# Optimization experiments

Measured on AMD Instinct MI355X. Metric: run time of the kernel, lower is better.

## Reference

```python
import jax, jax.numpy as jnp
import numpy as np

BS, LS, NWRD, D, H, NTGT, MC = 32, 512, 100000, 128, 512, 2048, 20
TEMP = 0.5  # gumbel-softmax temperature (self.last_t)
HLOSS_COEF = 0.03


def setup_inputs() -> dict:
    key = jax.random.key(0)
    ks = jax.random.split(key, 12)
    inp_word = jax.random.randint(ks[0], (BS, LS), 0, NWRD, dtype=jnp.int32)
    inp_char = jax.random.randint(ks[1], (BS, LS, MC), 0, 95, dtype=jnp.int32)
    inp_pos = jax.random.randint(ks[2], (BS, LS), 0, 50, dtype=jnp.int32)
    keyword_table = jax.random.bernoulli(ks[3], 0.1, (NWRD,))  # wid in keywords_set
    tgt_ids = jax.random.randint(ks[4], (NTGT,), 0, NWRD, dtype=jnp.int32)
    lut = jax.random.randint(ks[5], (NWRD, MC), 0, 95, dtype=jnp.int32)
    u = jax.random.uniform(ks[6], (BS, LS, NTGT), minval=1e-6, maxval=1.0 - 1e-6)
    gumbel = -jnp.log(-jnp.log(u))  # standard Gumbel(0,1) noise
    W = jax.random.normal(ks[7], (NWRD, D), dtype=jnp.float32) * 0.02
    W1 = jax.random.normal(ks[8], (D, H), dtype=jnp.float32) * (1.0 / np.sqrt(D))
    b1 = jnp.zeros((H,), jnp.float32)
    W2 = jax.random.normal(ks[9], (H, NTGT), dtype=jnp.float32) * (1.0 / np.sqrt(H))
    b2 = jnp.zeros((NTGT,), jnp.float32)
    return dict(inp_word=inp_word, inp_char=inp_char, inp_pos=inp_pos,
                keyword_table=keyword_table, tgt_ids=tgt_ids, lut=lut,
                gumbel=gumbel, W=W, W1=W1, b1=b1, W2=W2, b2=b2)


def reference(inp_word, inp_char, inp_pos, keyword_table, tgt_ids, lut,
              gumbel, W, W1, b1, W2, b2):
    # keyword membership mask (idx in the original; torch gathers only masked
    # spots -- here we compute densely and select with the mask, same math at
    # every masked position, identity elsewhere)
    mask = keyword_table[inp_word]                      # [bs, ls] bool

    x = W[inp_word]                                     # embed: [bs, ls, d]
    hdn = jax.nn.relu(jnp.einsum('bsd,dh->bsh', x, W1) + b1)
    logits = jnp.einsum('bsh,ht->bst', hdn, W2) + b2    # [bs, ls, ntgt]

    # log_p.masked_scatter_(idx, x.max(-1)[0])
    log_p = jnp.where(mask, logits.max(axis=-1), 0.0)

    # hloss: mean entropy over masked spots * 0.03
    lsm = jax.nn.log_softmax(logits, axis=-1)
    ent = -jnp.sum(jnp.exp(lsm) * lsm, axis=-1)         # [bs, ls]
    n_spots = jnp.maximum(mask.sum(), 1)
    loss_h = (ent * mask).sum() / n_spots * HLOSS_COEF

    # gumbel_softmax(x, t): softmax((logits + g) / t)
    sft = jax.nn.softmax((logits + gumbel) / TEMP, axis=-1)  # [bs, ls, ntgt]

    # hard pick mapped through tgtwords, scattered into word
    y = tgt_ids[jnp.argmax(sft, axis=-1)]               # [bs, ls]
    word = jnp.where(mask, y, inp_word)

    # soft embedding: sft @ word_emb_tgt, word_emb_tgt = W[tgt_ids]
    x_emb = jnp.einsum('bst,td->bsd', sft, W[tgt_ids])  # [bs, ls, d]
    word_emb = jnp.where(mask[..., None], x_emb, x)     # scatter into W[word]

    char = lut[word]                                    # word_to_char lookup

    return (mask.astype(jnp.float32), log_p, word, char, word_emb, loss_h)
```

## Files before the change

### kernel.cpp

```cpp
#include <hip/hip_runtime.h>
#include <cstdint>

#define R_TOT 16384
#define T_NT  2048
#define DD    128
#define HH    512
#define MC_   20
#define BR    32
#define STEPS 64
#define NBLK  (R_TOT / BR)

#define MASK_OFF 0
#define LOGP_OFF 16384
#define WORD_OFF 32768
#define CHAR_OFF 49152
#define EMB_OFF  376832
#define LOSS_OFF 2473984

#define X_OFF     0
#define HDN_OFF   2097152
#define HDNB_OFF  10485760
#define WT_OFF    14680064
#define WTT_OFF   14942208
#define W2T_OFF   15073280
#define W2TB_OFF  16121856
#define ENT_OFF   16646144
#define CNT_OFF   16647168

typedef __attribute__((ext_vector_type(8))) short short8v;
typedef __attribute__((ext_vector_type(4))) float f32x4;
typedef unsigned short ushort_t;

__device__ __forceinline__ ushort_t f2bf(float f) {
    union { float f; unsigned int u; } v; v.f = f;
    unsigned int r = v.u + 0x7FFFu + ((v.u >> 16) & 1u);
    return (ushort_t)(r >> 16);
}

__device__ __forceinline__ void stage16(const ushort_t* gsrc, ushort_t* ldst) {
    __builtin_amdgcn_global_load_lds(
        (const __attribute__((address_space(1))) unsigned int*)gsrc,
        (__attribute__((address_space(3))) unsigned int*)ldst, 16, 0, 0);
}

__global__ __launch_bounds__(256) void k1_gather(
    const int* __restrict__ inp_word, const int* __restrict__ tgt_ids,
    const float* __restrict__ W, float* __restrict__ x, float* __restrict__ wtgt)
{
    int row = blockIdx.x * 2 + (threadIdx.x >> 7);
    int d = threadIdx.x & 127;
    if (row < R_TOT) {
        int wsrc = inp_word[row];
        x[(size_t)row * DD + d] = W[(size_t)wsrc * DD + d];
    } else {
        int rr = row - R_TOT;
        if (rr < T_NT) {
            int wsrc = tgt_ids[rr];
            wtgt[(size_t)rr * DD + d] = W[(size_t)wsrc * DD + d];
        }
    }
}

__global__ __launch_bounds__(256) void k1b_wtgtT(
    const float* __restrict__ wtgt, ushort_t* __restrict__ wtgtT)
{
    __shared__ float tile[32][33];
    int tb = blockIdx.x * 32, db = blockIdx.y * 32;
    int lx = threadIdx.x & 31, ly = threadIdx.x >> 5;
    #pragma unroll
    for (int i = 0; i < 32; i += 8)
        tile[ly + i][lx] = wtgt[(size_t)(tb + ly + i) * DD + db + lx];
    __syncthreads();
    #pragma unroll
    for (int i = 0; i < 32; i += 8)
        wtgtT[(size_t)(db + ly + i) * T_NT + tb + lx] = f2bf(tile[lx][ly + i]);
}

__global__ __launch_bounds__(256) void k0_w2t(
    const float* __restrict__ W2, float* __restrict__ W2Tf, ushort_t* __restrict__ W2Tb)
{
    __shared__ float tile[32][33];
    int cb = blockIdx.x * 32, kb = blockIdx.y * 32;
    int lx = threadIdx.x & 31, ly = threadIdx.x >> 5;
    #pragma unroll
    for (int i = 0; i < 32; i += 8)
        tile[ly + i][lx] = W2[(size_t)(kb + ly + i) * T_NT + cb + lx];
    __syncthreads();
    #pragma unroll
    for (int i = 0; i < 32; i += 8) {
        int c = cb + ly + i, k = kb + lx;
        float v = tile[lx][ly + i];
        W2Tf[(size_t)c * HH + k] = v;
        W2Tb[(size_t)c * HH + k] = f2bf(v);
    }
}

__global__ __launch_bounds__(256) void k2_hdn(
    const float* __restrict__ x, const float* __restrict__ W1,
    const float* __restrict__ b1, float* __restrict__ hdn, ushort_t* __restrict__ hdnB)
{
    __shared__ float As[16][64];
    __shared__ float Bs[16][64];
    const int t = threadIdx.x;
    const int bm = blockIdx.x * 64;
    const int bn = blockIdx.y * 64;
    const int tx = t & 15, ty = t >> 4;
    float acc[4][4] = {};
    for (int k0 = 0; k0 < DD; k0 += 16) {
        {
            int m = t >> 2, kq = t & 3;
            float4 v = *(const float4*)(x + (size_t)(bm + m) * DD + k0 + kq * 4);
            As[kq * 4 + 0][m] = v.x; As[kq * 4 + 1][m] = v.y;
            As[kq * 4 + 2][m] = v.z; As[kq * 4 + 3][m] = v.w;
        }
        {
            int k = t >> 4, nq = t & 15;
            *(float4*)(&Bs[k][nq * 4]) =
                *(const float4*)(W1 + (size_t)(k0 + k) * HH + bn + nq * 4);
        }
        __syncthreads();
        #pragma unroll
        for (int k = 0; k < 16; ++k) {
            float a[4], b[4];
            #pragma unroll
            for (int i = 0; i < 4; i++) a[i] = As[k][ty * 4 + i];
            #pragma unroll
            for (int j = 0; j < 4; j++) b[j] = Bs[k][tx * 4 + j];
            #pragma unroll
            for (int i = 0; i < 4; i++)
                #pragma unroll
                for (int j = 0; j < 4; j++)
                    acc[i][j] = fmaf(a[i], b[j], acc[i][j]);
        }
        __syncthreads();
    }
    #pragma unroll
    for (int i = 0; i < 4; i++) {
        int m = bm + ty * 4 + i;
        int n = bn + tx * 4;
        float4 v;
        v.x = fmaxf(acc[i][0] + b1[n + 0], 0.f);
        v.y = fmaxf(acc[i][1] + b1[n + 1], 0.f);
        v.z = fmaxf(acc[i][2] + b1[n + 2], 0.f);
        v.w = fmaxf(acc[i][3] + b1[n + 3], 0.f);
        *(float4*)(hdn + (size_t)m * HH + n) = v;
        ushort4 hb;
        hb.x = f2bf(v.x); hb.y = f2bf(v.y); hb.z = f2bf(v.z); hb.w = f2bf(v.w);
        *(ushort4*)(hdnB + (size_t)m * HH + n) = hb;
    }
}

__global__ __launch_bounds__(256) void k3_fused(
    const ushort_t* __restrict__ hdnB, const float* __restrict__ hdn,
    const ushort_t* __restrict__ W2Tb, const float* __restrict__ W2Tf,
    const float* __restrict__ b2, const float* __restrict__ gumbel,
    const int* __restrict__ inp_word, const int* __restrict__ keyword_table,
    const int* __restrict__ tgt_ids, const int* __restrict__ lut,
    const float* __restrict__ x, const ushort_t* __restrict__ wtgtT,
    float* __restrict__ out, float* __restrict__ entP, float* __restrict__ cntP)
{
    __shared__ ushort_t wS[2][16384];
    __shared__ float pS[2 * 2 * 16 * 36];
    __shared__ float statC1[2 * 16 * 8];
    __shared__ int   candS[BR * 2];
    __shared__ float invs2S[BR], entS[BR];
    __shared__ int   mskS[BR];

    const int t = threadIdx.x;
    const int wid = t >> 6, lane = t & 63;
    const int Mgrp = wid >> 1, Cgrp = wid & 1;
    const int lrow = lane & 15, kgrp = lane >> 4;
    const int row0 = blockIdx.x * BR;
    const int rowA = row0 + Mgrp * 16 + lrow;
    const int c_local = Cgrp * 16 + lrow;

    short8v av[16];
    #pragma unroll
    for (int ks = 0; ks < 16; ++ks)
        av[ks] = *(const short8v*)(hdnB + (size_t)rowA * HH + ks * 32 + kgrp * 8);

    float m_[4], sE_[4], sEl_[4], s2_[4], a1_[4], a2_[4];
    int i1_[4], i2_[4];
    #pragma unroll
    for (int q = 0; q < 4; ++q) {
        m_[q] = -1e30f; sE_[q] = 0.f; sEl_[q] = 0.f; s2_[q] = 0.f;
        a1_[q] = -1e30f; a2_[q] = -1e30f; i1_[q] = 0; i2_[q] = 0;
    }
    f32x4 accpv[4];
    #pragma unroll
    for (int df = 0; df < 4; ++df) accpv[df] = (f32x4){0.f, 0.f, 0.f, 0.f};

    auto stage_tile = [&](int buf, int s_step) {
        const int col0 = s_step * 32;
        #pragma unroll
        for (int i = 0; i < 8; ++i) {
            int slot = wid * 512 + i * 64 + lane;
            int c = slot >> 6, kc = slot & 63;
            const ushort_t* gsrc = W2Tb + (size_t)(col0 + c) * HH + ((kc ^ (c & 7)) << 3);
            stage16(gsrc, &wS[buf][(size_t)(wid * 512 + i * 64) * 8]);
        }
    };

    stage_tile(0, 0);
    __syncthreads();

    const int dbase = Cgrp * 64 + lrow;

    for (int s = 0; s < STEPS; ++s) {
        const int buf = s & 1, par = s & 1;
        const int col = s * 32 + c_local;

        float g4[4];
        #pragma unroll
        for (int q = 0; q < 4; ++q)
            g4[q] = gumbel[(size_t)(row0 + Mgrp * 16 + kgrp * 4 + q) * T_NT + col];
        float b2v = b2[col];
        short8v bvf[4];
        #pragma unroll
        for (int df = 0; df < 4; ++df)
            bvf[df] = *(const short8v*)(wtgtT + (size_t)(dbase + df * 16) * T_NT + s * 32 + kgrp * 8);

        if (s + 1 < STEPS) stage_tile(buf ^ 1, s + 1);

        f32x4 acc = (f32x4){0.f, 0.f, 0.f, 0.f};
        #pragma unroll
        for (int ks = 0; ks < 16; ++ks) {
            int kc = ks * 4 + kgrp;
            const short8v bv = *(const short8v*)&wS[buf][c_local * 512 + ((kc ^ (c_local & 7)) << 3)];
            acc = __builtin_amdgcn_mfma_f32_16x16x32_bf16(av[ks], bv, acc, 0, 0, 0);
        }

        float* pT = &pS[(Mgrp * 2 + par) * 576];
        #pragma unroll
        for (int q = 0; q < 4; ++q) {
            float l = acc[q] + b2v;
            m_[q] = fmaxf(m_[q], l);
            float e1 = __expf(l);
            sE_[q] += e1; sEl_[q] = fmaf(e1, l, sEl_[q]);
            float a = l + g4[q];
            float p = __expf(2.0f * a);
            s2_[q] += p;
            if (a > a1_[q]) { a2_[q] = a1_[q]; i2_[q] = i1_[q]; a1_[q] = a; i1_[q] = col; }
            else if (a > a2_[q]) { a2_[q] = a; i2_[q] = col; }
            pT[(kgrp * 4 + q) * 36 + c_local] = p;
        }

        __syncthreads();

        {
            const float* pr = &pS[(Mgrp * 2 + par) * 576 + lrow * 36 + kgrp * 8];
            float4 pa = *(const float4*)(pr);
            float4 pb = *(const float4*)(pr + 4);
            short8v pav;
            pav[0] = (short)f2bf(pa.x); pav[1] = (short)f2bf(pa.y);
            pav[2] = (short)f2bf(pa.z); pav[3] = (short)f2bf(pa.w);
            pav[4] = (short)f2bf(pb.x); pav[5] = (short)f2bf(pb.y);
            pav[6] = (short)f2bf(pb.z); pav[7] = (short)f2bf(pb.w);
            #pragma unroll
            for (int df = 0; df < 4; ++df)
                accpv[df] = __builtin_amdgcn_mfma_f32_16x16x32_bf16(pav, bvf[df], accpv[df], 0, 0, 0);
        }
    }

    #pragma unroll
    for (int q = 0; q < 4; ++q) {
        #pragma unroll
        for (int mk = 1; mk < 16; mk <<= 1) {
            m_[q] = fmaxf(m_[q], __shfl_xor(m_[q], mk));
            sE_[q] += __shfl_xor(sE_[q], mk);
            sEl_[q] += __shfl_xor(sEl_[q], mk);
            s2_[q] += __shfl_xor(s2_[q], mk);
            float ob1 = __shfl_xor(a1_[q], mk); int oj1 = __shfl_xor(i1_[q], mk);
            float ob2 = __shfl_xor(a2_[q], mk); int oj2 = __shfl_xor(i2_[q], mk);
            if (ob1 > a1_[q] || (ob1 == a1_[q] && oj1 < i1_[q])) {
                if (a1_[q] > ob2 || (a1_[q] == ob2 && i1_[q] < oj2)) { a2_[q] = a1_[q]; i2_[q] = i1_[q]; }
                else { a2_[q] = ob2; i2_[q] = oj2; }
                a1_[q] = ob1; i1_[q] = oj1;
            } else {
                if (ob1 > a2_[q]) { a2_[q] = ob1; i2_[q] = oj1; }
            }
        }
    }

    if (Cgrp == 1 && lrow == 0) {
        #pragma unroll
        for (int q = 0; q < 4; ++q) {
            int r = kgrp * 4 + q;
            float* st = &statC1[(Mgrp * 16 + r) * 8];
            st[0] = m_[q]; st[1] = sE_[q]; st[2] = sEl_[q]; st[3] = s2_[q];
            st[4] = a1_[q]; st[5] = __int_as_float(i1_[q]);
            st[6] = a2_[q]; st[7] = __int_as_float(i2_[q]);
        }
    }
    __syncthreads();

    if (Cgrp == 0) {
        #pragma unroll
        for (int q = 0; q < 4; ++q) {
            int r = kgrp * 4 + q;
            const float* st = &statC1[(Mgrp * 16 + r) * 8];
            float bm = st[0], bsE = st[1], bsEl = st[2], bs2 = st[3];
            float b1v = st[4]; int j1 = __float_as_int(st[5]);
            float b2c = st[6]; int j2 = __float_as_int(st[7]);
            float m = fmaxf(m_[q], bm);
            float sE = sE_[q] + bsE, sEl = sEl_[q] + bsEl, s2 = s2_[q] + bs2;
            float a1 = a1_[q], a2 = a2_[q]; int i1 = i1_[q], i2 = i2_[q];
            if (b1v > a1 || (b1v == a1 && j1 < i1)) {
                if (a1 > b2c || (a1 == b2c && i1 < j2)) { a2 = a1; i2 = i1; }
                else { a2 = b2c; i2 = j2; }
                a1 = b1v; i1 = j1;
            } else {
                if (b1v > a2) { a2 = b1v; i2 = j1; }
            }
            if (lrow == 0) {
                int grow = row0 + Mgrp * 16 + r;
                int w_in = inp_word[grow];
                int msk = keyword_table[w_in] != 0;
                out[MASK_OFF + grow] = msk ? 1.0f : 0.0f;
                out[LOGP_OFF + grow] = msk ? m : 0.0f;
                invs2S[Mgrp * 16 + r] = 1.0f / s2;
                mskS[Mgrp * 16 + r] = msk;
                entS[Mgrp * 16 + r] = msk ? (__logf(sE) - sEl / sE) : 0.0f;
                candS[(Mgrp * 16 + r) * 2 + 0] = i1;
                candS[(Mgrp * 16 + r) * 2 + 1] = i2;
            }
        }
    }
    __syncthreads();

    #pragma unroll
    for (int df = 0; df < 4; ++df) {
        #pragma unroll
        for (int q = 0; q < 4; ++q) {
            int rl = Mgrp * 16 + kgrp * 4 + q;
            int grow = row0 + rl;
            int d = dbase + df * 16;
            float val = accpv[df][q] * invs2S[rl];
            if (!mskS[rl]) val = x[(size_t)grow * DD + d];
            out[EMB_OFF + (size_t)grow * DD + d] = val;
        }
    }

    for (int rr = wid * 8; rr < wid * 8 + 8; ++rr) {
        int grow = row0 + rr;
        int i1 = candS[rr * 2 + 0], i2 = candS[rr * 2 + 1];
        const float* hrow = hdn + (size_t)grow * HH;
        float4 h0 = *(const float4*)(hrow + lane * 8);
        float4 h1 = *(const float4*)(hrow + lane * 8 + 4);
        float v1, v2;
        {
            const float* wrow = W2Tf + (size_t)i1 * HH;
            float4 w0 = *(const float4*)(wrow + lane * 8);
            float4 w1 = *(const float4*)(wrow + lane * 8 + 4);
            float sdot = h0.x*w0.x + h0.y*w0.y + h0.z*w0.z + h0.w*w0.w
                       + h1.x*w1.x + h1.y*w1.y + h1.z*w1.z + h1.w*w1.w;
            #pragma unroll
            for (int mk = 1; mk < 64; mk <<= 1) sdot += __shfl_xor(sdot, mk);
            v1 = sdot + b2[i1] + gumbel[(size_t)grow * T_NT + i1];
        }
        {
            const float* wrow = W2Tf + (size_t)i2 * HH;
            float4 w0 = *(const float4*)(wrow + lane * 8);
            float4 w1 = *(const float4*)(wrow + lane * 8 + 4);
            float sdot = h0.x*w0.x + h0.y*w0.y + h0.z*w0.z + h0.w*w0.w
                       + h1.x*w1.x + h1.y*w1.y + h1.z*w1.z + h1.w*w1.w;
            #pragma unroll
            for (int mk = 1; mk < 64; mk <<= 1) sdot += __shfl_xor(sdot, mk);
            v2 = sdot + b2[i2] + gumbel[(size_t)grow * T_NT + i2];
        }
        int ibest = (v2 > v1 || (v2 == v1 && i2 < i1)) ? i2 : i1;
        int w_in = inp_word[grow];
        int msk = mskS[rr];
        int word = msk ? tgt_ids[ibest] : w_in;
        if (lane == 0) out[WORD_OFF + grow] = (float)word;
        if (lane < MC_)
            out[CHAR_OFF + (size_t)grow * MC_ + lane] = (float)lut[(size_t)word * MC_ + lane];
    }

    if (t == 0) {
        float es = 0.f; int cs = 0;
        #pragma unroll
        for (int r = 0; r < BR; r++) { es += entS[r]; cs += mskS[r]; }
        entP[blockIdx.x] = es;
        cntP[blockIdx.x] = (float)cs;
    }
}

__global__ __launch_bounds__(256) void k4_loss(
    const float* __restrict__ entP, const float* __restrict__ cntP, float* __restrict__ out)
{
    __shared__ float sE[256], sC[256];
    int t = threadIdx.x;
    float e = 0.f, c = 0.f;
    for (int i = t; i < NBLK; i += 256) { e += entP[i]; c += cntP[i]; }
    sE[t] = e; sC[t] = c;
    __syncthreads();
    for (int s = 128; s > 0; s >>= 1) {
        if (t < s) { sE[t] += sE[t + s]; sC[t] += sC[t + s]; }
        __syncthreads();
    }
    if (t == 0) {
        float ns = fmaxf(sC[0], 1.0f);
        out[LOSS_OFF] = 0.03f * sE[0] / ns;
    }
}

extern "C" void kernel_launch(void* const* d_in, const int* in_sizes, int n_in,
                              void* d_out, int out_size, void* d_ws, size_t ws_size,
                              hipStream_t stream) {
    const int* inp_word = (const int*)d_in[0];
    const int* keyword_table = (const int*)d_in[3];
    const int* tgt_ids = (const int*)d_in[4];
    const int* lut = (const int*)d_in[5];
    const float* gumbel = (const float*)d_in[6];
    const float* W = (const float*)d_in[7];
    const float* W1 = (const float*)d_in[8];
    const float* b1 = (const float*)d_in[9];
    const float* W2 = (const float*)d_in[10];
    const float* b2 = (const float*)d_in[11];
    float* out = (float*)d_out;

    float* wsf = (float*)d_ws;
    float* x = wsf + X_OFF;
    float* hdn = wsf + HDN_OFF;
    ushort_t* hdnB = (ushort_t*)(wsf + HDNB_OFF);
    float* wtgt = wsf + WT_OFF;
    ushort_t* wtgtT = (ushort_t*)(wsf + WTT_OFF);
    float* W2Tf = wsf + W2T_OFF;
    ushort_t* W2Tb = (ushort_t*)(wsf + W2TB_OFF);
    float* entP = wsf + ENT_OFF;
    float* cntP = wsf + CNT_OFF;

    k1_gather<<<(R_TOT + T_NT) / 2, 256, 0, stream>>>(inp_word, tgt_ids, W, x, wtgt);
    k1b_wtgtT<<<dim3(T_NT / 32, DD / 32), 256, 0, stream>>>(wtgt, wtgtT);
    k0_w2t<<<dim3(T_NT / 32, HH / 32), 256, 0, stream>>>(W2, W2Tf, W2Tb);
    k2_hdn<<<dim3(R_TOT / 64, HH / 64), 256, 0, stream>>>(x, W1, b1, hdn, hdnB);
    k3_fused<<<NBLK, 256, 0, stream>>>(hdnB, hdn, W2Tb, W2Tf, b2, gumbel,
                                       inp_word, keyword_table, tgt_ids, lut,
                                       x, wtgtT, out, entP, cntP);
    k4_loss<<<1, 256, 0, stream>>>(entP, cntP, out);
}
```

Baseline: 219.5 us.

## Prepack W2 and target embeddings into MFMA fragment layouts for the fused kernel

W2 and the gathered target embeddings are pre-packed in bf16 in the exact per-lane MFMA fragment order. The fused kernel can then stage contiguous tiles and read B fragments directly, without XOR swizzle address math or strided loads. The probability-times-embedding MFMA now runs per warp over its own 16 columns, zero-padding half of each K=32 input. This uses 8 accumulators covering all of D, and the two column-group partials are reduced through shared memory at the end. The logit MFMA chain is also split into four independent accumulators to improve ILP. The trade-off is more registers, wasted MFMA work on the padded inputs, and an extra reduction pass.

```diff
diff --git a/kernel.cpp b/kernel.cpp
--- a/kernel.cpp
+++ b/kernel.cpp
@@ -21,11 +21,11 @@
 #define HDN_OFF   2097152
 #define HDNB_OFF  10485760
 #define WT_OFF    14680064
-#define WTT_OFF   14942208
-#define W2T_OFF   15073280
-#define W2TB_OFF  16121856
-#define ENT_OFF   16646144
-#define CNT_OFF   16647168
+#define WTT4_OFF  14942208
+#define W2T_OFF   15204352
+#define W2P_OFF   16252928
+#define ENT_OFF   16777216
+#define CNT_OFF   16777728
 
 typedef __attribute__((ext_vector_type(8))) short short8v;
 typedef __attribute__((ext_vector_type(4))) float f32x4;
@@ -61,27 +61,33 @@
     }
 }
 
-__global__ __launch_bounds__(256) void k1b_wtgtT(
-    const float* __restrict__ wtgt, ushort_t* __restrict__ wtgtT)
+__global__ __launch_bounds__(256) void k1b_wtgtT4(
+    const float* __restrict__ wtgt, ushort_t* __restrict__ wtgtT4)
+{
+    const int js = blockIdx.x, t = threadIdx.x;
+    #pragma unroll
+    for (int i = 0; i < 4; ++i) {
+        int s = i * 256 + t;
+        int cs = s >> 9, rem = s & 511;
+        int df = rem >> 6, lane = rem & 63;
+        int lrow = lane & 15, kg = lane >> 4;
+        ushort_t* dst = wtgtT4 + (size_t)(((js * 2 + cs) * 8 + df) * 512 + lane * 8);
+        #pragma unroll
+        for (int j = 0; j < 8; ++j) {
+            dst[j] = (j < 4)
+                ? f2bf(wtgt[(size_t)(js * 32 + cs * 16 + kg * 4 + j) * DD + df * 16 + lrow])
+                : (ushort_t)0;
+        }
+    }
+}
+
+__global__ __launch_bounds__(256) void k0_w2t(
+    const float* __restrict__ W2, float* __restrict__ W2Tf, ushort_t* __restrict__ W2p)
 {
     __shared__ float tile[32][33];
-    int tb = blockIdx.x * 32, db = blockIdx.y * 32;
-    int lx = threadIdx.x & 31, ly = threadIdx.x >> 5;
-    #pragma unroll
-    for (int i = 0; i < 32; i += 8)
-        tile[ly + i][lx] = wtgt[(size_t)(tb + ly + i) * DD + db + lx];
-    __syncthreads();
-    #pragma unroll
-    for (int i = 0; i < 32; i += 8)
-        wtgtT[(size_t)(db + ly + i) * T_NT + tb + lx] = f2bf(tile[lx][ly + i]);
-}
-
-__global__ __launch_bounds__(256) void k0_w2t(
-    const float* __restrict__ W2, float* __restrict__ W2Tf, ushort_t* __restrict__ W2Tb)
-{
-    __shared__ float tile[32][33];
-    int cb = blockIdx.x * 32, kb = blockIdx.y * 32;
-    int lx = threadIdx.x & 31, ly = threadIdx.x >> 5;
+    const int js = blockIdx.x, ks = blockIdx.y;
+    const int cb = js * 32, kb = ks * 32;
+    const int lx = threadIdx.x & 31, ly = threadIdx.x >> 5;
     #pragma unroll
     for (int i = 0; i < 32; i += 8)
         tile[ly + i][lx] = W2[(size_t)(kb + ly + i) * T_NT + cb + lx];
@@ -89,9 +95,14 @@
     #pragma unroll
     for (int i = 0; i < 32; i += 8) {
         int c = cb + ly + i, k = kb + lx;
-        float v = tile[lx][ly + i];
-        W2Tf[(size_t)c * HH + k] = v;
-        W2Tb[(size_t)c * HH + k] = f2bf(v);
+        W2Tf[(size_t)c * HH + k] = tile[lx][ly + i];
+    }
+    if (threadIdx.x < 128) {
+        int c = threadIdx.x >> 2, kgrp = threadIdx.x & 3;
+        ushort_t* dst = W2p + (size_t)((js * 16 + ks) * 1024 + (c * 4 + kgrp) * 8);
+        #pragma unroll
+        for (int i = 0; i < 8; ++i)
+            dst[i] = f2bf(tile[kgrp * 8 + i][c]);
     }
 }
 
@@ -152,15 +163,15 @@
 
 __global__ __launch_bounds__(256) void k3_fused(
     const ushort_t* __restrict__ hdnB, const float* __restrict__ hdn,
-    const ushort_t* __restrict__ W2Tb, const float* __restrict__ W2Tf,
+    const ushort_t* __restrict__ W2p, const float* __restrict__ W2Tf,
     const float* __restrict__ b2, const float* __restrict__ gumbel,
     const int* __restrict__ inp_word, const int* __restrict__ keyword_table,
     const int* __restrict__ tgt_ids, const int* __restrict__ lut,
-    const float* __restrict__ x, const ushort_t* __restrict__ wtgtT,
+    const float* __restrict__ x, const ushort_t* __restrict__ wtgtT4,
     float* __restrict__ out, float* __restrict__ entP, float* __restrict__ cntP)
 {
-    __shared__ ushort_t wS[2][16384];
-    __shared__ float pS[2 * 2 * 16 * 36];
+    __shared__ ushort_t wS[2 * 16384];
+    __shared__ float pS[4][16 * 20];
     __shared__ float statC1[2 * 16 * 8];
     __shared__ int   candS[BR * 2];
     __shared__ float invs2S[BR], entS[BR];
@@ -172,12 +183,22 @@
     const int lrow = lane & 15, kgrp = lane >> 4;
     const int row0 = blockIdx.x * BR;
     const int rowA = row0 + Mgrp * 16 + lrow;
-    const int c_local = Cgrp * 16 + lrow;
 
     short8v av[16];
     #pragma unroll
     for (int ks = 0; ks < 16; ++ks)
         av[ks] = *(const short8v*)(hdnB + (size_t)rowA * HH + ks * 32 + kgrp * 8);
+
+    const ushort_t* wb = wS + ((Cgrp * 16 + lrow) * 4 + kgrp) * 8;
+
+    const float* gp0 = gumbel + (size_t)(row0 + Mgrp * 16 + kgrp * 4 + 0) * T_NT + Cgrp * 16 + lrow;
+    const float* gp1 = gp0 + T_NT;
+    const float* gp2 = gp1 + T_NT;
+    const float* gp3 = gp2 + T_NT;
+    const float* b2p = b2 + Cgrp * 16 + lrow;
+    const ushort_t* vtp = wtgtT4 + (size_t)Cgrp * 4096 + lane * 8;
+
+    float* pw = &pS[wid][0];
 
     float m_[4], sE_[4], sEl_[4], s2_[4], a1_[4], a2_[4];
     int i1_[4], i2_[4];
@@ -186,51 +207,51 @@
         m_[q] = -1e30f; sE_[q] = 0.f; sEl_[q] = 0.f; s2_[q] = 0.f;
         a1_[q] = -1e30f; a2_[q] = -1e30f; i1_[q] = 0; i2_[q] = 0;
     }
-    f32x4 accpv[4];
-    #pragma unroll
-    for (int df = 0; df < 4; ++df) accpv[df] = (f32x4){0.f, 0.f, 0.f, 0.f};
-
-    auto stage_tile = [&](int buf, int s_step) {
-        const int col0 = s_step * 32;
-        #pragma unroll
-        for (int i = 0; i < 8; ++i) {
-            int slot = wid * 512 + i * 64 + lane;
-            int c = slot >> 6, kc = slot & 63;
-            const ushort_t* gsrc = W2Tb + (size_t)(col0 + c) * HH + ((kc ^ (c & 7)) << 3);
-            stage16(gsrc, &wS[buf][(size_t)(wid * 512 + i * 64) * 8]);
-        }
-    };
-
-    stage_tile(0, 0);
+    f32x4 accpv[8];
+    #pragma unroll
+    for (int df = 0; df < 8; ++df) accpv[df] = (f32x4){0.f, 0.f, 0.f, 0.f};
+
+    {
+        const ushort_t* src = W2p + t * 8;
+        ushort_t* dst = wS + t * 8;
+        #pragma unroll
+        for (int i = 0; i < 8; ++i) stage16(src + i * 2048, dst + i * 2048);
+    }
     __syncthreads();
 
-    const int dbase = Cgrp * 64 + lrow;
+    int colv = Cgrp * 16 + lrow;
 
     for (int s = 0; s < STEPS; ++s) {
-        const int buf = s & 1, par = s & 1;
-        const int col = s * 32 + c_local;
-
-        float g4[4];
-        #pragma unroll
-        for (int q = 0; q < 4; ++q)
-            g4[q] = gumbel[(size_t)(row0 + Mgrp * 16 + kgrp * 4 + q) * T_NT + col];
-        float b2v = b2[col];
-        short8v bvf[4];
-        #pragma unroll
-        for (int df = 0; df < 4; ++df)
-            bvf[df] = *(const short8v*)(wtgtT + (size_t)(dbase + df * 16) * T_NT + s * 32 + kgrp * 8);
-
-        if (s + 1 < STEPS) stage_tile(buf ^ 1, s + 1);
-
-        f32x4 acc = (f32x4){0.f, 0.f, 0.f, 0.f};
-        #pragma unroll
-        for (int ks = 0; ks < 16; ++ks) {
-            int kc = ks * 4 + kgrp;
-            const short8v bv = *(const short8v*)&wS[buf][c_local * 512 + ((kc ^ (c_local & 7)) << 3)];
-            acc = __builtin_amdgcn_mfma_f32_16x16x32_bf16(av[ks], bv, acc, 0, 0, 0);
-        }
-
-        float* pT = &pS[(Mgrp * 2 + par) * 576];
+        const int buf = s & 1;
+
+        if (s + 1 < STEPS) {
+            const ushort_t* src = W2p + (size_t)(s + 1) * 16384 + t * 8;
+            ushort_t* dst = wS + (buf ^ 1) * 16384 + t * 8;
+            #pragma unroll
+            for (int i = 0; i < 8; ++i) stage16(src + i * 2048, dst + i * 2048);
+        }
+
+        float g0 = *gp0, g1 = *gp1, g2 = *gp2, g3 = *gp3;
+        gp0 += 32; gp1 += 32; gp2 += 32; gp3 += 32;
+        float b2v = *b2p; b2p += 32;
+        short8v bvf[8];
+        #pragma unroll
+        for (int df = 0; df < 8; ++df)
+            bvf[df] = *(const short8v*)(vtp + df * 512);
+        vtp += 8192;
+
+        const ushort_t* wbb = wb + buf * 16384;
+        f32x4 ac0 = (f32x4){0.f,0.f,0.f,0.f}, ac1 = ac0, ac2 = ac0, ac3 = ac0;
+        #pragma unroll
+        for (int ks = 0; ks < 16; ks += 4) {
+            ac0 = __builtin_amdgcn_mfma_f32_16x16x32_bf16(av[ks+0], *(const short8v*)(wbb + (ks+0)*1024), ac0, 0, 0, 0);
+            ac1 = __builtin_amdgcn_mfma_f32_16x16x32_bf16(av[ks+1], *(const short8v*)(wbb + (ks+1)*1024), ac1, 0, 0, 0);
+            ac2 = __builtin_amdgcn_mfma_f32_16x16x32_bf16(av[ks+2], *(const short8v*)(wbb + (ks+2)*1024), ac2, 0, 0, 0);
+            ac3 = __builtin_amdgcn_mfma_f32_16x16x32_bf16(av[ks+3], *(const short8v*)(wbb + (ks+3)*1024), ac3, 0, 0, 0);
+        }
+        f32x4 acc = (ac0 + ac1) + (ac2 + ac3);
+
+        float g4[4] = {g0, g1, g2, g3};
         #pragma unroll
         for (int q = 0; q < 4; ++q) {
             float l = acc[q] + b2v;
@@ -240,26 +261,24 @@
             float a = l + g4[q];
             float p = __expf(2.0f * a);
             s2_[q] += p;
-            if (a > a1_[q]) { a2_[q] = a1_[q]; i2_[q] = i1_[q]; a1_[q] = a; i1_[q] = col; }
-            else if (a > a2_[q]) { a2_[q] = a; i2_[q] = col; }
-            pT[(kgrp * 4 + q) * 36 + c_local] = p;
+            if (a > a1_[q]) { a2_[q] = a1_[q]; i2_[q] = i1_[q]; a1_[q] = a; i1_[q] = colv; }
+            else if (a > a2_[q]) { a2_[q] = a; i2_[q] = colv; }
+            pw[(kgrp * 4 + q) * 20 + lrow] = p;
+        }
+
+        {
+            float4 p4 = *(const float4*)(pw + lrow * 20 + kgrp * 4);
+            short8v pav;
+            pav[0] = (short)f2bf(p4.x); pav[1] = (short)f2bf(p4.y);
+            pav[2] = (short)f2bf(p4.z); pav[3] = (short)f2bf(p4.w);
+            pav[4] = 0; pav[5] = 0; pav[6] = 0; pav[7] = 0;
+            #pragma unroll
+            for (int df = 0; df < 8; ++df)
+                accpv[df] = __builtin_amdgcn_mfma_f32_16x16x32_bf16(pav, bvf[df], accpv[df], 0, 0, 0);
         }
 
         __syncthreads();
-
-        {
-            const float* pr = &pS[(Mgrp * 2 + par) * 576 + lrow * 36 + kgrp * 8];
-            float4 pa = *(const float4*)(pr);
-            float4 pb = *(const float4*)(pr + 4);
-            short8v pav;
-            pav[0] = (short)f2bf(pa.x); pav[1] = (short)f2bf(pa.y);
-            pav[2] = (short)f2bf(pa.z); pav[3] = (short)f2bf(pa.w);
-            pav[4] = (short)f2bf(pb.x); pav[5] = (short)f2bf(pb.y);
-            pav[6] = (short)f2bf(pb.z); pav[7] = (short)f2bf(pb.w);
-            #pragma unroll
-            for (int df = 0; df < 4; ++df)
-                accpv[df] = __builtin_amdgcn_mfma_f32_16x16x32_bf16(pav, bvf[df], accpv[df], 0, 0, 0);
-        }
+        colv += 32;
     }
 
     #pragma unroll
@@ -285,12 +304,19 @@
     if (Cgrp == 1 && lrow == 0) {
         #pragma unroll
         for (int q = 0; q < 4; ++q) {
-            int r = kgrp * 4 + q;
-            float* st = &statC1[(Mgrp * 16 + r) * 8];
+            float* st = &statC1[(Mgrp * 16 + kgrp * 4 + q) * 8];
             st[0] = m_[q]; st[1] = sE_[q]; st[2] = sEl_[q]; st[3] = s2_[q];
             st[4] = a1_[q]; st[5] = __int_as_float(i1_[q]);
             st[6] = a2_[q]; st[7] = __int_as_float(i2_[q]);
         }
+    }
+    float* scr = (float*)wS;
+    if (Cgrp == 1) {
+        #pragma unroll
+        for (int df = 0; df < 8; ++df)
+            #pragma unroll
+            for (int q = 0; q < 4; ++q)
+                scr[Mgrp * 2048 + (kgrp * 4 + q) * 128 + df * 16 + lrow] = accpv[df][q];
     }
     __syncthreads();
 
@@ -300,48 +326,56 @@
             int r = kgrp * 4 + q;
             const float* st = &statC1[(Mgrp * 16 + r) * 8];
             float bm = st[0], bsE = st[1], bsEl = st[2], bs2 = st[3];
-            float b1v = st[4]; int j1 = __float_as_int(st[5]);
-            float b2c = st[6]; int j2 = __float_as_int(st[7]);
+            float ob1 = st[4]; int oj1 = __float_as_int(st[5]);
+            float ob2 = st[6]; int oj2 = __float_as_int(st[7]);
             float m = fmaxf(m_[q], bm);
             float sE = sE_[q] + bsE, sEl = sEl_[q] + bsEl, s2 = s2_[q] + bs2;
             float a1 = a1_[q], a2 = a2_[q]; int i1 = i1_[q], i2 = i2_[q];
-            if (b1v > a1 || (b1v == a1 && j1 < i1)) {
-                if (a1 > b2c || (a1 == b2c && i1 < j2)) { a2 = a1; i2 = i1; }
-                else { a2 = b2c; i2 = j2; }
-                a1 = b1v; i1 = j1;
+            if (ob1 > a1 || (ob1 == a1 && oj1 < i1)) {
+                if (a1 > ob2 || (a1 == ob2 && i1 < oj2)) { a2 = a1; i2 = i1; }
+                else { a2 = ob2; i2 = oj2; }
+                a1 = ob1; i1 = oj1;
             } else {
-                if (b1v > a2) { a2 = b1v; i2 = j1; }
+                if (ob1 > a2) { a2 = ob1; i2 = oj1; }
             }
             if (lrow == 0) {
-                int grow = row0 + Mgrp * 16 + r;
+                int rl = Mgrp * 16 + r;
+                int grow = row0 + rl;
                 int w_in = inp_word[grow];
                 int msk = keyword_table[w_in] != 0;
                 out[MASK_OFF + grow] = msk ? 1.0f : 0.0f;
                 out[LOGP_OFF + grow] = msk ? m : 0.0f;
-                invs2S[Mgrp * 16 + r] = 1.0f / s2;
-                mskS[Mgrp * 16 + r] = msk;
-                entS[Mgrp * 16 + r] = msk ? (__logf(sE) - sEl / sE) : 0.0f;
-                candS[(Mgrp * 16 + r) * 2 + 0] = i1;
-                candS[(Mgrp * 16 + r) * 2 + 1] = i2;
+                invs2S[rl] = 1.0f / s2;
+                mskS[rl] = msk;
+                entS[rl] = msk ? (__logf(sE) - sEl / sE) : 0.0f;
+                candS[rl * 2 + 0] = i1;
+                candS[rl * 2 + 1] = i2;
             }
         }
+        #pragma unroll
+        for (int df = 0; df < 8; ++df)
+            #pragma unroll
+            for (int q = 0; q < 4; ++q)
+                accpv[df][q] += scr[Mgrp * 2048 + (kgrp * 4 + q) * 128 + df * 16 + lrow];
     }
     __syncthreads();
 
-    #pragma unroll
-    for (int df = 0; df < 4; ++df) {
-        #pragma unroll
-        for (int q = 0; q < 4; ++q) {
-            int rl = Mgrp * 16 + kgrp * 4 + q;
-            int grow = row0 + rl;
-            int d = dbase + df * 16;
-            float val = accpv[df][q] * invs2S[rl];
-            if (!mskS[rl]) val = x[(size_t)grow * DD + d];
-            out[EMB_OFF + (size_t)grow * DD + d] = val;
-        }
-    }
-
-    for (int rr = wid * 8; rr < wid * 8 + 8; ++rr) {
+    if (Cgrp == 0) {
+        #pragma unroll
+        for (int df = 0; df < 8; ++df) {
+            #pragma unroll
+            for (int q = 0; q < 4; ++q) {
+                int rl = Mgrp * 16 + kgrp * 4 + q;
+                int grow = row0 + rl;
+                int d = df * 16 + lrow;
+                float val = accpv[df][q] * invs2S[rl];
+                if (!mskS[rl]) val = x[(size_t)grow * DD + d];
+                out[EMB_OFF + (size_t)grow * DD + d] = val;
+            }
+        }
+    }
+
+    for (int rr = wid; rr < BR; rr += 4) {
         int grow = row0 + rr;
         int i1 = candS[rr * 2 + 0], i2 = candS[rr * 2 + 1];
         const float* hrow = hdn + (size_t)grow * HH;
@@ -425,18 +459,18 @@
     float* hdn = wsf + HDN_OFF;
     ushort_t* hdnB = (ushort_t*)(wsf + HDNB_OFF);
     float* wtgt = wsf + WT_OFF;
-    ushort_t* wtgtT = (ushort_t*)(wsf + WTT_OFF);
+    ushort_t* wtgtT4 = (ushort_t*)(wsf + WTT4_OFF);
     float* W2Tf = wsf + W2T_OFF;
-    ushort_t* W2Tb = (ushort_t*)(wsf + W2TB_OFF);
+    ushort_t* W2p = (ushort_t*)(wsf + W2P_OFF);
     float* entP = wsf + ENT_OFF;
     float* cntP = wsf + CNT_OFF;
 
     k1_gather<<<(R_TOT + T_NT) / 2, 256, 0, stream>>>(inp_word, tgt_ids, W, x, wtgt);
-    k1b_wtgtT<<<dim3(T_NT / 32, DD / 32), 256, 0, stream>>>(wtgt, wtgtT);
-    k0_w2t<<<dim3(T_NT / 32, HH / 32), 256, 0, stream>>>(W2, W2Tf, W2Tb);
+    k1b_wtgtT4<<<64, 256, 0, stream>>>(wtgt, wtgtT4);
+    k0_w2t<<<dim3(T_NT / 32, HH / 32), 256, 0, stream>>>(W2, W2Tf, W2p);
     k2_hdn<<<dim3(R_TOT / 64, HH / 64), 256, 0, stream>>>(x, W1, b1, hdn, hdnB);
-    k3_fused<<<NBLK, 256, 0, stream>>>(hdnB, hdn, W2Tb, W2Tf, b2, gumbel,
+    k3_fused<<<NBLK, 256, 0, stream>>>(hdnB, hdn, W2p, W2Tf, b2, gumbel,
                                        inp_word, keyword_table, tgt_ids, lut,
-                                       x, wtgtT, out, entP, cntP);
+                                       x, wtgtT4, out, entP, cntP);
     k4_loss<<<1, 256, 0, stream>>>(entP, cntP, out);
 }
```

After: 215.8 us. Within noise of the previous version (-1.7%).
